# Performance work log

Hardware: AMD Instinct MI355X
Metric: run time of the kernel (lower is better)

Reference implementation:

```python
import jax, jax.numpy as jnp
import numpy as np

N = 524288          # query points
N_COMP = 36         # sdf_n_comp
GRID = 512          # cubic grid resolution
SDF_DIM = 256
APP_DIM = 128
MAT_MODE = [(0, 1), (0, 2), (1, 2)]
VEC_MODE = [2, 1, 0]
PE_FREQS = (1.0, 2.0, 4.0)  # sdf_multires=3, log-sampled 2^0..2^2


def _pos_enc(x):
    # NeRF embedder, include_input=True: [x, sin(f x), cos(f x) per freq]
    outs = [x]
    for f in PE_FREQS:
        outs.append(jnp.sin(x * f))
        outs.append(jnp.cos(x * f))
    return jnp.concatenate(outs, axis=-1)  # (N, 21)


def _bilinear_plane(plane, gx, gy):
    # plane: (C, H, W); gx indexes W, gy indexes H; align_corners=True
    C, H, W = plane.shape
    px = (gx + 1.0) * 0.5 * (W - 1)
    py = (gy + 1.0) * 0.5 * (H - 1)
    x0 = jnp.clip(jnp.floor(px), 0, W - 2).astype(jnp.int32)
    y0 = jnp.clip(jnp.floor(py), 0, H - 2).astype(jnp.int32)
    x1, y1 = x0 + 1, y0 + 1
    wx = px - x0
    wy = py - y0
    f00 = plane[:, y0, x0]  # (C, N)
    f01 = plane[:, y0, x1]
    f10 = plane[:, y1, x0]
    f11 = plane[:, y1, x1]
    return (f00 * (1 - wx) + f01 * wx) * (1 - wy) + (f10 * (1 - wx) + f11 * wx) * wy


def _linear_line(line, g):
    # line: (C, L); g in [-1, 1]; align_corners=True
    C, L = line.shape
    p = (g + 1.0) * 0.5 * (L - 1)
    i0 = jnp.clip(jnp.floor(p), 0, L - 2).astype(jnp.int32)
    w = p - i0
    return line[:, i0] * (1 - w) + line[:, i0 + 1] * w  # (C, N)


def setup_inputs() -> dict:
    key = jax.random.key(0)
    ks = jax.random.split(key, 6)
    xyz = jax.random.uniform(ks[0], (N, 3), dtype=jnp.float32)  # points in aabb [0,1]^3
    planes = jax.random.normal(ks[1], (3, N_COMP, GRID, GRID), dtype=jnp.float32) * 0.1
    lines = jax.random.normal(ks[2], (3, N_COMP, GRID), dtype=jnp.float32) * 0.1
    in_ch = N_COMP * 3 + 21  # 129
    W1 = jax.random.normal(ks[3], (in_ch, SDF_DIM), dtype=jnp.float32) * (np.sqrt(2.0) / np.sqrt(SDF_DIM))
    b1 = jnp.zeros((SDF_DIM,), dtype=jnp.float32)
    W2 = jax.random.normal(ks[4], (SDF_DIM, 1 + APP_DIM), dtype=jnp.float32) * 0.0001 + np.sqrt(np.pi) / np.sqrt(SDF_DIM)
    b2 = jnp.full((1 + APP_DIM,), -0.2, dtype=jnp.float32)  # init_radius bias
    return {"xyz": xyz, "planes": planes, "lines": lines, "W1": W1, "b1": b1, "W2": W2, "b2": b2}


def reference(xyz, planes, lines, W1, b1, W2, b2):
    # contraction: normalize aabb [0,1]^3 -> [-1,1]
    xn = 2.0 * xyz - 1.0  # (N, 3)
    # sampling coords are detached in the original (coordinate_plane.detach())
    xs = jax.lax.stop_gradient(xn)
    feats = []
    for i in range(3):
        m0, m1 = MAT_MODE[i]
        pfeat = _bilinear_plane(planes[i], xs[:, m0], xs[:, m1])  # (C, N)
        lfeat = _linear_line(lines[i], xs[:, VEC_MODE[i]])        # (C, N)
        feats.append(pfeat * lfeat)
    feat = jnp.concatenate(feats, axis=0).T  # (N, 3C)
    pe = _pos_enc(xn)                         # (N, 21)
    h = jnp.concatenate([feat, pe], axis=-1)  # (N, 129)
    h = jax.nn.softplus(100.0 * (h @ W1 + b1)) / 100.0  # Softplus(beta=100)
    out = h @ W2 + b2  # (N, 1 + app_dim); out[..., :1] is the SDF
    return out
```

## Files before the change

### kernel.cpp

```cpp
#include <hip/hip_runtime.h>
#include <math.h>

typedef unsigned short u16;
typedef unsigned int u32;
typedef __attribute__((ext_vector_type(2))) u32 u32x2;
typedef __attribute__((ext_vector_type(8))) short short8;
typedef __attribute__((ext_vector_type(4))) float f32x4;
typedef __attribute__((ext_vector_type(2))) float f32x2;

#define OFF_LINES_T 62914560u
#define OFF_W1S     63037440u
#define OFF_W2S     63119360u
#define WS_NEEDED   63217664u

__device__ __forceinline__ float bf_lo(u32 u){ union{u32 i;float f;} v; v.i = u << 16; return v.f; }
__device__ __forceinline__ float bf_hi(u32 u){ union{u32 i;float f;} v; v.i = u & 0xffff0000u; return v.f; }
__device__ __forceinline__ u16 f2bf(float f){ union{float f;u32 i;} v; v.f=f; u32 i=v.i; return (u16)((i + 0x7fffu + ((i>>16)&1u)) >> 16); }
__device__ __forceinline__ u32 pack2bf(float lo, float hi){ return (u32)f2bf(lo) | ((u32)f2bf(hi)<<16); }
__device__ __forceinline__ u32 pack2bf_fast(float lo, float hi){
  return __builtin_amdgcn_perm(__float_as_uint(hi) + 0x8000u,
                               __float_as_uint(lo) + 0x8000u, 0x07060302u);
}
__device__ __forceinline__ u16 f2bf_fast(float f){ return (u16)((__float_as_uint(f) + 0x8000u) >> 16); }

__device__ __forceinline__ int map_k1(int kp){
  if (kp < 120){ int g = kp/40, r = kp - g*40; return (r<36) ? g*36 + r : -1; }
  if (kp < 141) return kp - 12;
  return -1;
}

#define NB_TP 15360
#define NB_TL 30
#define NB_W1 20
#define NB_W2 24
__global__ void k_pre(const float* __restrict__ planes, const float* __restrict__ lines,
                      const float* __restrict__ W1, const float* __restrict__ W2,
                      u16* __restrict__ pt, u16* __restrict__ lt,
                      u16* __restrict__ w1s, u16* __restrict__ w2s){
  const int b = blockIdx.x;
  const int tid = threadIdx.x;
  if (b < NB_TP){
    int m = b*256 + tid;
    int tt = m/5, cc = m - tt*5;
    int i = tt >> 18;
    int yx = tt & 262143;
    const float* src = planes + (size_t)i*9437184 + yx;
    int cbase = cc*8;
    float v[8];
#pragma unroll
    for (int e=0;e<8;e++) v[e] = 0.f;
    if (cc < 4){
#pragma unroll
      for (int e=0;e<8;e++) v[e] = src[(size_t)(cbase+e)*262144];
    } else {
#pragma unroll
      for (int e=0;e<4;e++) v[e] = src[(size_t)(32+e)*262144];
    }
    uint4 o; o.x=pack2bf(v[0],v[1]); o.y=pack2bf(v[2],v[3]); o.z=pack2bf(v[4],v[5]); o.w=pack2bf(v[6],v[7]);
    *reinterpret_cast<uint4*>(pt + (size_t)m*8) = o;
  } else if (b < NB_TP+NB_TL){
    int m = (b-NB_TP)*256 + tid;
    int tt = m/5, cc = m - tt*5;
    int i = tt >> 9, g = tt & 511;
    const float* src = lines + (size_t)i*18432 + g;
    int cbase = cc*8;
    float v[8];
#pragma unroll
    for (int e=0;e<8;e++) v[e] = 0.f;
    if (cc < 4){
#pragma unroll
      for (int e=0;e<8;e++) v[e] = src[(size_t)(cbase+e)*512];
    } else {
#pragma unroll
      for (int e=0;e<4;e++) v[e] = src[(size_t)(32+e)*512];
    }
    uint4 o; o.x=pack2bf(v[0],v[1]); o.y=pack2bf(v[2],v[3]); o.z=pack2bf(v[4],v[5]); o.w=pack2bf(v[6],v[7]);
    *reinterpret_cast<uint4*>(lt + (size_t)m*8) = o;
  } else if (b < NB_TP+NB_TL+NB_W1){
    int t = (b-(NB_TP+NB_TL))*256 + tid;
    int lane = t & 63;
    int fid = t >> 6;
    int nt = fid/5, kt = fid - nt*5;
    int n = nt*16 + (lane & 15);
    int kb = kt*32 + (lane >> 4)*8;
    float v[8];
#pragma unroll
    for (int j=0;j<8;j++){ int k = map_k1(kb+j); v[j] = (k>=0) ? W1[k*256+n] : 0.f; }
    uint4 o; o.x=pack2bf(v[0],v[1]); o.y=pack2bf(v[2],v[3]); o.z=pack2bf(v[4],v[5]); o.w=pack2bf(v[6],v[7]);
    *reinterpret_cast<uint4*>(w1s + (size_t)t*8) = o;
  } else {
    int t = (b-(NB_TP+NB_TL+NB_W1))*256 + tid;
    int lane = t & 63;
    int fid = t >> 6;
    int kb = (fid & 7)*32 + (lane >> 4)*8;
    int n = (fid >> 3)*16 + (lane & 15);
    float v[8];
#pragma unroll
    for (int j=0;j<8;j++){ int k = kb+j; v[j] = (n<129) ? W2[k*129+n] : 0.f; }
    uint4 o; o.x=pack2bf(v[0],v[1]); o.y=pack2bf(v[2],v[3]); o.z=pack2bf(v[4],v[5]); o.w=pack2bf(v[6],v[7]);
    *reinterpret_cast<uint4*>(w2s + (size_t)t*8) = o;
  }
}

__device__ __forceinline__ f32x2 bfx2(u32 u){
  f32x2 r;
  r.x = __uint_as_float(u << 16);
  r.y = __uint_as_float(u & 0xffff0000u);
  return r;
}

__device__ __forceinline__ u32 blend2(u32 u00,u32 u01,u32 u10,u32 u11,u32 g0,u32 g1,
                                      float w00,float w01,float w10,float w11,
                                      float v0,float v1){
  f32x2 pf = bfx2(u00)*w00 + bfx2(u01)*w01 + bfx2(u10)*w10 + bfx2(u11)*w11;
  f32x2 lf = bfx2(g0)*v0 + bfx2(g1)*v1;
  f32x2 r  = pf*lf;
  return pack2bf_fast(r.x, r.y);
}

#define FSTRIDE 168
#define HSTRIDE 264

__global__ void __launch_bounds__(256, 5) k_main(
    const float* __restrict__ xyz, const u16* __restrict__ pt,
    const u16* __restrict__ lt, const u16* __restrict__ w1s,
    const u16* __restrict__ w2s, const float* __restrict__ b1,
    const float* __restrict__ b2, float* __restrict__ out)
{
  __shared__ __align__(16) u16 smem[32*HSTRIDE];
  const int tid = threadIdx.x;
  const int p = tid >> 3, q = tid & 7;
  const int gp = blockIdx.x*32 + p;
  const float u0 = xyz[gp*3], u1 = xyz[gp*3+1], u2 = xyz[gp*3+2];
  const float xn0 = 2.f*u0-1.f, xn1 = 2.f*u1-1.f, xn2 = 2.f*u2-1.f;

  if (q < 6){
    const int i = q >> 1, part = q & 1;
    float gxv, gyv, gzv;
    if      (i==0){ gxv=xn0; gyv=xn1; gzv=xn2; }
    else if (i==1){ gxv=xn0; gyv=xn2; gzv=xn1; }
    else          { gxv=xn1; gyv=xn2; gzv=xn0; }
    float px=(gxv+1.0f)*0.5f*511.0f, py=(gyv+1.0f)*0.5f*511.0f, pz=(gzv+1.0f)*0.5f*511.0f;
    float fx=fminf(fmaxf(floorf(px),0.f),510.f);
    float fy=fminf(fmaxf(floorf(py),0.f),510.f);
    float fz=fminf(fmaxf(floorf(pz),0.f),510.f);
    int ix=(int)fx, iy=(int)fy, iz=(int)fz;
    float wx=px-fx, wy=py-fy, wz=pz-fz;
    const float cwx = 1.f-wx, cwy = 1.f-wy;
    const float w00 = cwx*cwy, w01 = wx*cwy, w10 = cwx*wy, w11 = wx*wy;
    const float v0 = 1.f-wz, v1 = wz;
    const int nch = part ? 2 : 3;
    const u16* tb = pt + (size_t)((i<<18)+(iy<<9)+ix)*40 + part*24;
    const u16* lb = lt + (size_t)((i<<9)+iz)*40 + part*24;
    u16* dst = smem + p*FSTRIDE + i*40 + part*24;
#pragma unroll
    for (int ch=0; ch<3; ch++){
      if (ch < nch){
        uint4 a00 = *reinterpret_cast<const uint4*>(tb + ch*8);
        uint4 a01 = *reinterpret_cast<const uint4*>(tb + 40 + ch*8);
        uint4 a10 = *reinterpret_cast<const uint4*>(tb + 20480 + ch*8);
        uint4 a11 = *reinterpret_cast<const uint4*>(tb + 20520 + ch*8);
        uint4 e0  = *reinterpret_cast<const uint4*>(lb + ch*8);
        uint4 e1  = *reinterpret_cast<const uint4*>(lb + 40 + ch*8);
        uint4 o;
        o.x = blend2(a00.x,a01.x,a10.x,a11.x,e0.x,e1.x, w00,w01,w10,w11,v0,v1);
        o.y = blend2(a00.y,a01.y,a10.y,a11.y,e0.y,e1.y, w00,w01,w10,w11,v0,v1);
        o.z = blend2(a00.z,a01.z,a10.z,a11.z,e0.z,e1.z, w00,w01,w10,w11,v0,v1);
        o.w = blend2(a00.w,a01.w,a10.w,a11.w,e0.w,e1.w, w00,w01,w10,w11,v0,v1);
        *reinterpret_cast<uint4*>(dst + ch*8) = o;
      }
    }
  } else if (q == 6){
    float v[20];
    v[0]=xn0; v[1]=xn1; v[2]=xn2;
    v[3]=__sinf(xn0);      v[4]=__sinf(xn1);      v[5]=__sinf(xn2);
    v[6]=__cosf(xn0);      v[7]=__cosf(xn1);      v[8]=__cosf(xn2);
    v[9]=__sinf(2.f*xn0);  v[10]=__sinf(2.f*xn1); v[11]=__sinf(2.f*xn2);
    v[12]=__cosf(2.f*xn0); v[13]=__cosf(2.f*xn1); v[14]=__cosf(2.f*xn2);
    v[15]=__sinf(4.f*xn0); v[16]=__sinf(4.f*xn1); v[17]=__sinf(4.f*xn2);
    v[18]=__cosf(4.f*xn0); v[19]=__cosf(4.f*xn1);
    u16* dst = smem + p*FSTRIDE + 120;
#pragma unroll
    for (int c=0; c<10; c++)
      *reinterpret_cast<u32*>(dst + c*2) = pack2bf_fast(v[c*2], v[c*2+1]);
  } else {
    u16* dst = smem + p*FSTRIDE + 140;
    *reinterpret_cast<u32*>(dst) = pack2bf_fast(__cosf(4.f*xn2), 0.f);
#pragma unroll
    for (int c=1; c<10; c++)
      *reinterpret_cast<u32*>(dst + c*2) = 0u;
  }
  __syncthreads();

  const int lane = tid & 63;
  const int w = tid >> 6;
  const int lm = lane & 15;
  const int quad = lane >> 4;
  const f32x4 zero = {0.f,0.f,0.f,0.f};
  f32x4 acc[2][4];
#pragma unroll
  for (int mt=0; mt<2; mt++)
#pragma unroll
    for (int nt=0; nt<4; nt++) acc[mt][nt] = zero;

#pragma unroll
  for (int kt=0; kt<5; kt++){
    short8 a[2];
#pragma unroll
    for (int mt=0; mt<2; mt++)
      a[mt] = *reinterpret_cast<const short8*>(smem + (mt*16 + lm)*FSTRIDE + kt*32 + quad*8);
    short8 b[4];
#pragma unroll
    for (int nt=0; nt<4; nt++)
      b[nt] = *reinterpret_cast<const short8*>(w1s + (size_t)(((w*4+nt)*5 + kt)*64 + lane)*8);
#pragma unroll
    for (int mt=0; mt<2; mt++)
#pragma unroll
      for (int nt=0; nt<4; nt++)
        acc[mt][nt] = __builtin_amdgcn_mfma_f32_16x16x32_bf16(a[mt], b[nt], acc[mt][nt], 0,0,0);
  }
  __syncthreads();

#pragma unroll
  for (int nt=0; nt<4; nt++){
    int col = w*64 + nt*16 + lm;
    float bias = b1[col];
#pragma unroll
    for (int mt=0; mt<2; mt++){
#pragma unroll
      for (int r=0; r<4; r++){
        float xv = acc[mt][nt][r] + bias;
        float z = 100.f*xv;
        float y = (z > 15.f) ? xv : __logf(1.f + __expf(z))*0.01f;
        int row = mt*16 + quad*4 + r;
        smem[row*HSTRIDE + col] = f2bf_fast(y);
      }
    }
  }
  __builtin_amdgcn_sched_barrier(0);
  __syncthreads();

#pragma unroll
  for (int mt=0; mt<2; mt++)
#pragma unroll
    for (int nt=0; nt<3; nt++) acc[mt][nt] = zero;

#pragma unroll
  for (int kt=0; kt<8; kt++){
    short8 a[2];
#pragma unroll
    for (int mt=0; mt<2; mt++)
      a[mt] = *reinterpret_cast<const short8*>(smem + (mt*16 + lm)*HSTRIDE + kt*32 + quad*8);
    short8 b[3];
#pragma unroll
    for (int nt=0; nt<3; nt++){
      int ntg = w*3 + nt;
      b[nt] = *reinterpret_cast<const short8*>(w2s + (size_t)((ntg*8 + kt)*64 + lane)*8);
    }
#pragma unroll
    for (int mt=0; mt<2; mt++)
#pragma unroll
      for (int nt=0; nt<3; nt++)
        acc[mt][nt] = __builtin_amdgcn_mfma_f32_16x16x32_bf16(a[mt], b[nt], acc[mt][nt], 0,0,0);
  }

#pragma unroll
  for (int nt=0; nt<3; nt++){
    int j = (w*3 + nt)*16 + lm;
    if (j < 129){
      float bias = b2[j];
#pragma unroll
      for (int mt=0; mt<2; mt++){
#pragma unroll
        for (int r=0; r<4; r++){
          int row = mt*16 + quad*4 + r;
          out[(size_t)(blockIdx.x*32 + row)*129 + j] = acc[mt][nt][r] + bias;
        }
      }
    }
  }
}

extern "C" void kernel_launch(void* const* d_in, const int* in_sizes, int n_in,
                              void* d_out, int out_size, void* d_ws, size_t ws_size,
                              hipStream_t stream) {
  const float* xyz    = (const float*)d_in[0];
  const float* planes = (const float*)d_in[1];
  const float* lines  = (const float*)d_in[2];
  const float* W1     = (const float*)d_in[3];
  const float* b1     = (const float*)d_in[4];
  const float* W2     = (const float*)d_in[5];
  const float* b2     = (const float*)d_in[6];
  if (ws_size < (size_t)WS_NEEDED) return;

  u16* pt  = (u16*)((char*)d_ws);
  u16* lt  = (u16*)((char*)d_ws + OFF_LINES_T);
  u16* w1s = (u16*)((char*)d_ws + OFF_W1S);
  u16* w2s = (u16*)((char*)d_ws + OFF_W2S);

  k_pre<<<NB_TP+NB_TL+NB_W1+NB_W2, 256, 0, stream>>>(planes, lines, W1, W2, pt, lt, w1s, w2s);
  k_main<<<16384, 256, 0, stream>>>(xyz, pt, lt, w1s, w2s, b1, b2, (float*)d_out);
}
```

Before: 598.8 us.

## Halve points per block to 16 and spread gather across 16 threads per point

Each block now handles 16 points instead of 32, with 16 threads per point. Fifteen threads each gather one 8-channel chunk and the sixteenth computes the positional encoding. The MFMA tiles drop from two M-tiles to one, which shrinks accumulators and shared memory, and the launch bound is raised to 6 for occupancy. The cost is that each W1/W2 fragment loaded from global is reused for only one M-tile, doubling weight traffic per point and the number of blocks.

```diff
diff --git a/kernel.cpp b/kernel.cpp
--- a/kernel.cpp
+++ b/kernel.cpp
@@ -121,21 +121,21 @@
 #define FSTRIDE 168
 #define HSTRIDE 264
 
-__global__ void __launch_bounds__(256, 5) k_main(
+__global__ void __launch_bounds__(256, 6) k_main(
     const float* __restrict__ xyz, const u16* __restrict__ pt,
     const u16* __restrict__ lt, const u16* __restrict__ w1s,
     const u16* __restrict__ w2s, const float* __restrict__ b1,
     const float* __restrict__ b2, float* __restrict__ out)
 {
-  __shared__ __align__(16) u16 smem[32*HSTRIDE];
+  __shared__ __align__(16) u16 smem[16*HSTRIDE];
   const int tid = threadIdx.x;
-  const int p = tid >> 3, q = tid & 7;
-  const int gp = blockIdx.x*32 + p;
+  const int p = tid >> 4, q = tid & 15;
+  const int gp = blockIdx.x*16 + p;
   const float u0 = xyz[gp*3], u1 = xyz[gp*3+1], u2 = xyz[gp*3+2];
   const float xn0 = 2.f*u0-1.f, xn1 = 2.f*u1-1.f, xn2 = 2.f*u2-1.f;
 
-  if (q < 6){
-    const int i = q >> 1, part = q & 1;
+  if (q < 15){
+    const int i = q/5, cc = q - i*5;
     float gxv, gyv, gzv;
     if      (i==0){ gxv=xn0; gyv=xn1; gzv=xn2; }
     else if (i==1){ gxv=xn0; gyv=xn2; gzv=xn1; }
@@ -149,45 +149,36 @@
     const float cwx = 1.f-wx, cwy = 1.f-wy;
     const float w00 = cwx*cwy, w01 = wx*cwy, w10 = cwx*wy, w11 = wx*wy;
     const float v0 = 1.f-wz, v1 = wz;
-    const int nch = part ? 2 : 3;
-    const u16* tb = pt + (size_t)((i<<18)+(iy<<9)+ix)*40 + part*24;
-    const u16* lb = lt + (size_t)((i<<9)+iz)*40 + part*24;
-    u16* dst = smem + p*FSTRIDE + i*40 + part*24;
-#pragma unroll
-    for (int ch=0; ch<3; ch++){
-      if (ch < nch){
-        uint4 a00 = *reinterpret_cast<const uint4*>(tb + ch*8);
-        uint4 a01 = *reinterpret_cast<const uint4*>(tb + 40 + ch*8);
-        uint4 a10 = *reinterpret_cast<const uint4*>(tb + 20480 + ch*8);
-        uint4 a11 = *reinterpret_cast<const uint4*>(tb + 20520 + ch*8);
-        uint4 e0  = *reinterpret_cast<const uint4*>(lb + ch*8);
-        uint4 e1  = *reinterpret_cast<const uint4*>(lb + 40 + ch*8);
-        uint4 o;
-        o.x = blend2(a00.x,a01.x,a10.x,a11.x,e0.x,e1.x, w00,w01,w10,w11,v0,v1);
-        o.y = blend2(a00.y,a01.y,a10.y,a11.y,e0.y,e1.y, w00,w01,w10,w11,v0,v1);
-        o.z = blend2(a00.z,a01.z,a10.z,a11.z,e0.z,e1.z, w00,w01,w10,w11,v0,v1);
-        o.w = blend2(a00.w,a01.w,a10.w,a11.w,e0.w,e1.w, w00,w01,w10,w11,v0,v1);
-        *reinterpret_cast<uint4*>(dst + ch*8) = o;
-      }
-    }
-  } else if (q == 6){
-    float v[20];
+    const u16* tb = pt + (size_t)((i<<18)+(iy<<9)+ix)*40 + cc*8;
+    const u16* lb = lt + (size_t)((i<<9)+iz)*40 + cc*8;
+    uint4 a00 = *reinterpret_cast<const uint4*>(tb);
+    uint4 a01 = *reinterpret_cast<const uint4*>(tb + 40);
+    uint4 a10 = *reinterpret_cast<const uint4*>(tb + 20480);
+    uint4 a11 = *reinterpret_cast<const uint4*>(tb + 20520);
+    uint4 e0  = *reinterpret_cast<const uint4*>(lb);
+    uint4 e1  = *reinterpret_cast<const uint4*>(lb + 40);
+    uint4 o;
+    o.x = blend2(a00.x,a01.x,a10.x,a11.x,e0.x,e1.x, w00,w01,w10,w11,v0,v1);
+    o.y = blend2(a00.y,a01.y,a10.y,a11.y,e0.y,e1.y, w00,w01,w10,w11,v0,v1);
+    o.z = blend2(a00.z,a01.z,a10.z,a11.z,e0.z,e1.z, w00,w01,w10,w11,v0,v1);
+    o.w = blend2(a00.w,a01.w,a10.w,a11.w,e0.w,e1.w, w00,w01,w10,w11,v0,v1);
+    *reinterpret_cast<uint4*>(smem + p*FSTRIDE + i*40 + cc*8) = o;
+  } else {
+    float v[21];
     v[0]=xn0; v[1]=xn1; v[2]=xn2;
     v[3]=__sinf(xn0);      v[4]=__sinf(xn1);      v[5]=__sinf(xn2);
     v[6]=__cosf(xn0);      v[7]=__cosf(xn1);      v[8]=__cosf(xn2);
     v[9]=__sinf(2.f*xn0);  v[10]=__sinf(2.f*xn1); v[11]=__sinf(2.f*xn2);
     v[12]=__cosf(2.f*xn0); v[13]=__cosf(2.f*xn1); v[14]=__cosf(2.f*xn2);
     v[15]=__sinf(4.f*xn0); v[16]=__sinf(4.f*xn1); v[17]=__sinf(4.f*xn2);
-    v[18]=__cosf(4.f*xn0); v[19]=__cosf(4.f*xn1);
+    v[18]=__cosf(4.f*xn0); v[19]=__cosf(4.f*xn1); v[20]=__cosf(4.f*xn2);
     u16* dst = smem + p*FSTRIDE + 120;
 #pragma unroll
     for (int c=0; c<10; c++)
       *reinterpret_cast<u32*>(dst + c*2) = pack2bf_fast(v[c*2], v[c*2+1]);
-  } else {
-    u16* dst = smem + p*FSTRIDE + 140;
-    *reinterpret_cast<u32*>(dst) = pack2bf_fast(__cosf(4.f*xn2), 0.f);
-#pragma unroll
-    for (int c=1; c<10; c++)
+    *reinterpret_cast<u32*>(dst + 20) = pack2bf_fast(v[20], 0.f);
+#pragma unroll
+    for (int c=11; c<20; c++)
       *reinterpret_cast<u32*>(dst + c*2) = 0u;
   }
   __syncthreads();
@@ -197,27 +188,20 @@
   const int lm = lane & 15;
   const int quad = lane >> 4;
   const f32x4 zero = {0.f,0.f,0.f,0.f};
-  f32x4 acc[2][4];
-#pragma unroll
-  for (int mt=0; mt<2; mt++)
-#pragma unroll
-    for (int nt=0; nt<4; nt++) acc[mt][nt] = zero;
+  f32x4 acc[4];
+#pragma unroll
+  for (int nt=0; nt<4; nt++) acc[nt] = zero;
 
 #pragma unroll
   for (int kt=0; kt<5; kt++){
-    short8 a[2];
-#pragma unroll
-    for (int mt=0; mt<2; mt++)
-      a[mt] = *reinterpret_cast<const short8*>(smem + (mt*16 + lm)*FSTRIDE + kt*32 + quad*8);
+    short8 a = *reinterpret_cast<const short8*>(smem + lm*FSTRIDE + kt*32 + quad*8);
     short8 b[4];
 #pragma unroll
     for (int nt=0; nt<4; nt++)
       b[nt] = *reinterpret_cast<const short8*>(w1s + (size_t)(((w*4+nt)*5 + kt)*64 + lane)*8);
 #pragma unroll
-    for (int mt=0; mt<2; mt++)
-#pragma unroll
-      for (int nt=0; nt<4; nt++)
-        acc[mt][nt] = __builtin_amdgcn_mfma_f32_16x16x32_bf16(a[mt], b[nt], acc[mt][nt], 0,0,0);
+    for (int nt=0; nt<4; nt++)
+      acc[nt] = __builtin_amdgcn_mfma_f32_16x16x32_bf16(a, b[nt], acc[nt], 0,0,0);
   }
   __syncthreads();
 
@@ -226,31 +210,23 @@
     int col = w*64 + nt*16 + lm;
     float bias = b1[col];
 #pragma unroll
-    for (int mt=0; mt<2; mt++){
-#pragma unroll
-      for (int r=0; r<4; r++){
-        float xv = acc[mt][nt][r] + bias;
-        float z = 100.f*xv;
-        float y = (z > 15.f) ? xv : __logf(1.f + __expf(z))*0.01f;
-        int row = mt*16 + quad*4 + r;
-        smem[row*HSTRIDE + col] = f2bf_fast(y);
-      }
+    for (int r=0; r<4; r++){
+      float xv = acc[nt][r] + bias;
+      float z = 100.f*xv;
+      float y = (z > 15.f) ? xv : __logf(1.f + __expf(z))*0.01f;
+      int row = quad*4 + r;
+      smem[row*HSTRIDE + col] = f2bf_fast(y);
     }
   }
   __builtin_amdgcn_sched_barrier(0);
   __syncthreads();
 
 #pragma unroll
-  for (int mt=0; mt<2; mt++)
-#pragma unroll
-    for (int nt=0; nt<3; nt++) acc[mt][nt] = zero;
+  for (int nt=0; nt<3; nt++) acc[nt] = zero;
 
 #pragma unroll
   for (int kt=0; kt<8; kt++){
-    short8 a[2];
-#pragma unroll
-    for (int mt=0; mt<2; mt++)
-      a[mt] = *reinterpret_cast<const short8*>(smem + (mt*16 + lm)*HSTRIDE + kt*32 + quad*8);
+    short8 a = *reinterpret_cast<const short8*>(smem + lm*HSTRIDE + kt*32 + quad*8);
     short8 b[3];
 #pragma unroll
     for (int nt=0; nt<3; nt++){
@@ -258,10 +234,8 @@
       b[nt] = *reinterpret_cast<const short8*>(w2s + (size_t)((ntg*8 + kt)*64 + lane)*8);
     }
 #pragma unroll
-    for (int mt=0; mt<2; mt++)
-#pragma unroll
-      for (int nt=0; nt<3; nt++)
-        acc[mt][nt] = __builtin_amdgcn_mfma_f32_16x16x32_bf16(a[mt], b[nt], acc[mt][nt], 0,0,0);
+    for (int nt=0; nt<3; nt++)
+      acc[nt] = __builtin_amdgcn_mfma_f32_16x16x32_bf16(a, b[nt], acc[nt], 0,0,0);
   }
 
 #pragma unroll
@@ -270,12 +244,9 @@
     if (j < 129){
       float bias = b2[j];
 #pragma unroll
-      for (int mt=0; mt<2; mt++){
-#pragma unroll
-        for (int r=0; r<4; r++){
-          int row = mt*16 + quad*4 + r;
-          out[(size_t)(blockIdx.x*32 + row)*129 + j] = acc[mt][nt][r] + bias;
-        }
+      for (int r=0; r<4; r++){
+        int row = quad*4 + r;
+        out[(size_t)(blockIdx.x*16 + row)*129 + j] = acc[nt][r] + bias;
       }
     }
   }
@@ -299,5 +270,5 @@
   u16* w2s = (u16*)((char*)d_ws + OFF_W2S);
 
   k_pre<<<NB_TP+NB_TL+NB_W1+NB_W2, 256, 0, stream>>>(planes, lines, W1, W2, pt, lt, w1s, w2s);
-  k_main<<<16384, 256, 0, stream>>>(xyz, pt, lt, w1s, w2s, b1, b2, (float*)d_out);
-}
+  k_main<<<32768, 256, 0, stream>>>(xyz, pt, lt, w1s, w2s, b1, b2, (float*)d_out);
+}
```

Result: slower. 622.7 us (+4.0%).
